# Performance work log

Hardware: AMD Instinct MI355X
Metric: run time of the kernel (lower is better)

## Reference

```python
import jax, jax.numpy as jnp
import numpy as np

DIM = 256
HEADS = 8
WH, WW = 7, 7
N = WH * WW
B_ = 2048


def _relative_position_index(wh, ww):
    coords = np.stack(np.meshgrid(np.arange(wh), np.arange(ww), indexing='ij'))  # (2,wh,ww)
    cf = coords.reshape(2, -1)  # (2, N)
    rel = cf[:, :, None] - cf[:, None, :]  # (2, N, N)
    rel = rel.transpose(1, 2, 0).astype(np.int32)
    rel[:, :, 0] += wh - 1
    rel[:, :, 1] += ww - 1
    rel[:, :, 0] *= 2 * ww - 1
    return rel.sum(-1)  # (N, N) int32


def setup_inputs() -> dict:
    key = jax.random.key(0)
    ks = jax.random.split(key, 7)
    return {
        'x1': jax.random.normal(ks[0], (B_, N, DIM), jnp.float32),
        'x2': jax.random.normal(ks[1], (B_, N, DIM), jnp.float32),
        'qkv_w': jax.random.normal(ks[2], (3 * DIM, DIM), jnp.float32) * 0.02,
        'qkv_b': jax.random.normal(ks[3], (3 * DIM,), jnp.float32) * 0.02,
        'proj_w': jax.random.normal(ks[4], (DIM, DIM), jnp.float32) * 0.02,
        'proj_b': jax.random.normal(ks[5], (DIM,), jnp.float32) * 0.02,
        'rpb_table': jax.random.normal(ks[6], ((2 * WH - 1) * (2 * WW - 1), HEADS), jnp.float32) * 0.02,
        'rel_index': jnp.asarray(_relative_position_index(WH, WW)),
    }


def reference(x1, x2, qkv_w, qkv_b, proj_w, proj_b, rpb_table, rel_index):
    B, n, C = x1.shape
    H = HEADS
    d = C // H
    scale = d ** (-0.5)

    def qkv(x):
        y = x @ qkv_w.T + qkv_b  # (B, N, 3C)
        y = y.reshape(B, n, 3, H, d).transpose(2, 0, 3, 1, 4)  # (3, B, H, N, d)
        return y[0], y[1], y[2]

    q1, _, _ = qkv(x1)
    _, k2, v2 = qkv(x2)

    attn = jnp.einsum('bhnd,bhmd->bhnm', q1 * scale, k2)  # (B, H, N, N)
    bias = rpb_table[rel_index]  # (N, N, H)
    attn = attn + bias.transpose(2, 0, 1)[None]  # broadcast over batch
    attn = jax.nn.softmax(attn, axis=-1)

    out = jnp.einsum('bhnm,bhmd->bhnd', attn, v2)  # (B, H, N, d)
    out = out.transpose(0, 2, 1, 3).reshape(B, n, C)
    return out @ proj_w.T + proj_b
```

## Files before the change

### kernel.cpp

```cpp
#include <hip/hip_runtime.h>
#include <hip/hip_bf16.h>

#define NTOK 49
#define NP 64
#define CDIM 256
#define NH 8
#define SCALE 0.17677669529663687f

#define SX_BYTES 32768
#define SV_BYTES 32768
#define SP_BYTES 16384

using f32x4  = __attribute__((ext_vector_type(4))) float;
using bf16x8 = __attribute__((ext_vector_type(8))) short;

__device__ __forceinline__ unsigned f2bf_u(float f) {
  union { float f; unsigned u; } c; c.f = f;
  return (c.u + 0x7fffu + ((c.u >> 16) & 1u)) >> 16;
}
__device__ __forceinline__ unsigned pk2(float a, float b) {
  return f2bf_u(a) | (f2bf_u(b) << 16);
}

__device__ __forceinline__ int sx_b(int row, int col) {
  return (row * 512 + col * 2) ^ ((row & 7) << 4);
}
__device__ __forceinline__ int sv_b(int feat, int tok) {
  return (feat * 128 + tok * 2) ^ ((feat & 7) << 4);
}
__device__ __forceinline__ int sp_b(int w, int row, int key) {
  return w * 2048 + ((row * 128 + key * 2) ^ ((row & 7) << 4));
}
__device__ __forceinline__ int so_b(int row, int col) {
  return (row * 512 + col * 4) ^ ((row & 7) << 4);
}

__global__ void prep_kernel(const float* __restrict__ qkv_w, const float* __restrict__ qkv_b,
                            const float* __restrict__ proj_w,
                            const float* __restrict__ rpb, const int* __restrict__ rel,
                            short* __restrict__ wqkv, short* __restrict__ wp,
                            float* __restrict__ bias_s, float* __restrict__ bias_att) {
  int i = blockIdx.x * 256 + threadIdx.x;
  if (i < 768 * 256) {
    int j = i >> 8;
    float v = qkv_w[i] * (j < 256 ? SCALE : 1.0f);
    wqkv[i] = (short)f2bf_u(v);
    return;
  }
  i -= 768 * 256;
  if (i < 256 * 256) { wp[i] = (short)f2bf_u(proj_w[i]); return; }
  i -= 256 * 256;
  if (i < 768) { bias_s[i] = qkv_b[i] * (i < 256 ? SCALE : 1.0f); return; }
  i -= 768;
  if (i < NH * NP * NP) {
    int h = i >> 12, rem = i & 4095, r = rem >> 6, c = rem & 63;
    float v;
    if (c >= NTOK)      v = -1e30f;
    else if (r >= NTOK) v = 0.0f;
    else                v = rpb[rel[r * NTOK + c] * NH + h];
    bias_att[i] = v;
  }
}

__device__ __forceinline__ void gemm32(const char* sxc, const short* __restrict__ wg,
                                       const float* __restrict__ bias,
                                       f32x4 acc[4][2], int w, int lr, int lg) {
  const short* wr0 = wg + (w * 32 + lr) * CDIM + lg * 8;
  const short* wr1 = wg + (w * 32 + 16 + lr) * CDIM + lg * 8;
  const float bv0 = bias[w * 32 + lr];
  const float bv1 = bias[w * 32 + 16 + lr];
  #pragma unroll
  for (int rt = 0; rt < 4; ++rt) {
    #pragma unroll
    for (int r = 0; r < 4; ++r) { acc[rt][0][r] = bv0; acc[rt][1][r] = bv1; }
  }
  #pragma unroll
  for (int k = 0; k < 8; ++k) {
    const bf16x8 b0 = *(const bf16x8*)(wr0 + k * 32);
    const bf16x8 b1 = *(const bf16x8*)(wr1 + k * 32);
    #pragma unroll
    for (int rt = 0; rt < 4; ++rt) {
      const bf16x8 af = *(const bf16x8*)(sxc + sx_b(rt * 16 + lr, k * 32 + lg * 8));
      acc[rt][0] = __builtin_amdgcn_mfma_f32_16x16x32_bf16(af, b0, acc[rt][0], 0, 0, 0);
      acc[rt][1] = __builtin_amdgcn_mfma_f32_16x16x32_bf16(af, b1, acc[rt][1], 0, 0, 0);
    }
  }
}

template <int NT>
__device__ __forceinline__ void stage_x(char* sxc, const float* __restrict__ xg, int tid) {
  #pragma unroll
  for (int it = 0; it < 4096 / NT; ++it) {
    const int i = tid + it * NT;
    const int row = i >> 6, c4 = i & 63;
    uint2 pkv = make_uint2(0u, 0u);
    if (row < NTOK) {
      const float4 v = *(const float4*)(xg + row * CDIM + c4 * 4);
      pkv.x = pk2(v.x, v.y); pkv.y = pk2(v.z, v.w);
    }
    *(uint2*)(sxc + sx_b(row, c4 * 4)) = pkv;
  }
}

#define IMG_STRIDE 98304

__global__ __launch_bounds__(512) __attribute__((amdgpu_waves_per_eu(4, 4)))
void qkv_kernel(const float* __restrict__ x1, const float* __restrict__ x2,
                const short* __restrict__ wqkv, const float* __restrict__ bias_s,
                char* __restrict__ img) {
  extern __shared__ char ldsc[];
  char* sxc = ldsc;
  char* stc = ldsc + 32768;

  const int tid = threadIdx.x;
  const int w = tid >> 6, lane = tid & 63;
  const int lr = lane & 15, lg = lane >> 4;
  const int b = blockIdx.x;
  char* wsb = img + (size_t)b * IMG_STRIDE;

  f32x4 acc[4][2];

  stage_x<512>(sxc, x1 + (size_t)b * NTOK * CDIM, tid);
  __syncthreads();

  gemm32(sxc, wqkv, bias_s, acc, w, lr, lg);
  #pragma unroll
  for (int rt = 0; rt < 4; ++rt)
    #pragma unroll
    for (int ct = 0; ct < 2; ++ct)
      #pragma unroll
      for (int r = 0; r < 4; ++r)
        *(short*)(stc + sx_b(rt * 16 + lg * 4 + r, w * 32 + ct * 16 + lr)) =
            (short)f2bf_u(acc[rt][ct][r]);
  __syncthreads();

  #pragma unroll
  for (int it = 0; it < 4; ++it) {
    const int i = tid + it * 512;
    *(float4*)(wsb + i * 16) = *(const float4*)(stc + i * 16);
  }
  stage_x<512>(sxc, x2 + (size_t)b * NTOK * CDIM, tid);
  __syncthreads();

  gemm32(sxc, wqkv + 512 * CDIM, bias_s + 512, acc, w, lr, lg);
  #pragma unroll
  for (int rt = 0; rt < 4; ++rt)
    #pragma unroll
    for (int ct = 0; ct < 2; ++ct) {
      uint2 pkv = make_uint2(pk2(acc[rt][ct][0], acc[rt][ct][1]),
                             pk2(acc[rt][ct][2], acc[rt][ct][3]));
      *(uint2*)(stc + sv_b(w * 32 + ct * 16 + lr, rt * 16 + lg * 4)) = pkv;
    }
  __syncthreads();

  #pragma unroll
  for (int it = 0; it < 4; ++it) {
    const int i = tid + it * 512;
    *(float4*)(wsb + 65536 + i * 16) = *(const float4*)(stc + i * 16);
  }
  gemm32(sxc, wqkv + 256 * CDIM, bias_s + 256, acc, w, lr, lg);
  __syncthreads();

  #pragma unroll
  for (int rt = 0; rt < 4; ++rt)
    #pragma unroll
    for (int ct = 0; ct < 2; ++ct)
      #pragma unroll
      for (int r = 0; r < 4; ++r)
        *(short*)(stc + sx_b(rt * 16 + lg * 4 + r, w * 32 + ct * 16 + lr)) =
            (short)f2bf_u(acc[rt][ct][r]);
  __syncthreads();

  #pragma unroll
  for (int it = 0; it < 4; ++it) {
    const int i = tid + it * 512;
    *(float4*)(wsb + 32768 + i * 16) = *(const float4*)(stc + i * 16);
  }
}

__global__ __launch_bounds__(256) __attribute__((amdgpu_waves_per_eu(4, 4)))
void attnproj_kernel(const char* __restrict__ img, const short* __restrict__ wp,
                     const float* __restrict__ proj_b, const float* __restrict__ bias_att,
                     float* __restrict__ out) {
  extern __shared__ char ldsc[];
  char* soc = ldsc;
  char* spc = ldsc + 32768;

  const int tid = threadIdx.x;
  const int w = tid >> 6, lane = tid & 63;
  const int lr = lane & 15, lg = lane >> 4;
  const int b = blockIdx.x;
  const char* qimg = img + (size_t)b * IMG_STRIDE;
  const char* kimg = qimg + 32768;
  const char* vimg = qimg + 65536;

  #pragma unroll
  for (int hh = 0; hh < 2; ++hh) {
    const int h = w * 2 + hh;
    bf16x8 kb[4];
    #pragma unroll
    for (int ct = 0; ct < 4; ++ct)
      kb[ct] = *(const bf16x8*)(kimg + sx_b(ct * 16 + lr, h * 32 + lg * 8));
    bf16x8 vb[2][2];
    #pragma unroll
    for (int kk = 0; kk < 2; ++kk)
      #pragma unroll
      for (int jt = 0; jt < 2; ++jt)
        vb[kk][jt] = *(const bf16x8*)(vimg + sv_b(h * 32 + jt * 16 + lr, kk * 32 + lg * 8));
    const float* bh = bias_att + h * NP * NP;

    #pragma unroll
    for (int qt = 0; qt < 4; ++qt) {
      const bf16x8 qa = *(const bf16x8*)(qimg + sx_b(qt * 16 + lr, h * 32 + lg * 8));
      f32x4 s[4];
      #pragma unroll
      for (int ct = 0; ct < 4; ++ct) {
        f32x4 sb;
        #pragma unroll
        for (int r = 0; r < 4; ++r) sb[r] = bh[(qt * 16 + lg * 4 + r) * NP + ct * 16 + lr];
        s[ct] = __builtin_amdgcn_mfma_f32_16x16x32_bf16(qa, kb[ct], sb, 0, 0, 0);
      }
      float mx[4], si[4];
      #pragma unroll
      for (int r = 0; r < 4; ++r) {
        float m = fmaxf(fmaxf(s[0][r], s[1][r]), fmaxf(s[2][r], s[3][r]));
        m = fmaxf(m, __shfl_xor(m, 1, 64));
        m = fmaxf(m, __shfl_xor(m, 2, 64));
        m = fmaxf(m, __shfl_xor(m, 4, 64));
        m = fmaxf(m, __shfl_xor(m, 8, 64));
        mx[r] = m;
      }
      #pragma unroll
      for (int ct = 0; ct < 4; ++ct)
        #pragma unroll
        for (int r = 0; r < 4; ++r)
          s[ct][r] = __expf(s[ct][r] - mx[r]);
      #pragma unroll
      for (int r = 0; r < 4; ++r) {
        float t = s[0][r] + s[1][r] + s[2][r] + s[3][r];
        t += __shfl_xor(t, 1, 64);
        t += __shfl_xor(t, 2, 64);
        t += __shfl_xor(t, 4, 64);
        t += __shfl_xor(t, 8, 64);
        si[r] = __builtin_amdgcn_rcpf(t);
      }
      #pragma unroll
      for (int ct = 0; ct < 4; ++ct)
        #pragma unroll
        for (int r = 0; r < 4; ++r)
          *(short*)(spc + sp_b(w, lg * 4 + r, ct * 16 + lr)) =
              (short)f2bf_u(s[ct][r] * si[r]);
      f32x4 oq[2];
      #pragma unroll
      for (int jt = 0; jt < 2; ++jt) { oq[jt][0] = 0; oq[jt][1] = 0; oq[jt][2] = 0; oq[jt][3] = 0; }
      #pragma unroll
      for (int kk = 0; kk < 2; ++kk) {
        const bf16x8 pa = *(const bf16x8*)(spc + sp_b(w, lr, kk * 32 + lg * 8));
        #pragma unroll
        for (int jt = 0; jt < 2; ++jt)
          oq[jt] = __builtin_amdgcn_mfma_f32_16x16x32_bf16(pa, vb[kk][jt], oq[jt], 0, 0, 0);
      }
      #pragma unroll
      for (int jt = 0; jt < 2; ++jt)
        #pragma unroll
        for (int r = 0; r < 4; ++r)
          *(short*)(soc + sx_b(qt * 16 + lg * 4 + r, h * 32 + jt * 16 + lr)) =
              (short)f2bf_u(oq[jt][r]);
    }
  }
  __syncthreads();

  float* og = out + (size_t)b * NTOK * CDIM;
  #pragma unroll
  for (int p = 0; p < 2; ++p) {
    const int c0 = w * 64 + p * 32;
    const short* wr0 = wp + (c0 + lr) * CDIM + lg * 8;
    const short* wr1 = wp + (c0 + 16 + lr) * CDIM + lg * 8;
    const float bv0 = proj_b[c0 + lr];
    const float bv1 = proj_b[c0 + 16 + lr];
    f32x4 acc[4][2];
    #pragma unroll
    for (int rt = 0; rt < 4; ++rt)
      #pragma unroll
      for (int r = 0; r < 4; ++r) { acc[rt][0][r] = bv0; acc[rt][1][r] = bv1; }
    #pragma unroll
    for (int k = 0; k < 8; ++k) {
      const bf16x8 b0 = *(const bf16x8*)(wr0 + k * 32);
      const bf16x8 b1 = *(const bf16x8*)(wr1 + k * 32);
      #pragma unroll
      for (int rt = 0; rt < 4; ++rt) {
        const bf16x8 af = *(const bf16x8*)(soc + sx_b(rt * 16 + lr, k * 32 + lg * 8));
        acc[rt][0] = __builtin_amdgcn_mfma_f32_16x16x32_bf16(af, b0, acc[rt][0], 0, 0, 0);
        acc[rt][1] = __builtin_amdgcn_mfma_f32_16x16x32_bf16(af, b1, acc[rt][1], 0, 0, 0);
      }
    }
    #pragma unroll
    for (int rt = 0; rt < 4; ++rt)
      #pragma unroll
      for (int r = 0; r < 4; ++r) {
        const int row = rt * 16 + lg * 4 + r;
        if (row < NTOK) {
          #pragma unroll
          for (int ct = 0; ct < 2; ++ct)
            og[row * CDIM + c0 + ct * 16 + lr] = acc[rt][ct][r];
        }
      }
  }
}

__global__ __launch_bounds__(512) __attribute__((amdgpu_waves_per_eu(4, 4)))
void fused_attn(const float* __restrict__ x1, const float* __restrict__ x2,
                const short* __restrict__ wqkv, const float* __restrict__ bias_s,
                const short* __restrict__ wp, const float* __restrict__ proj_b,
                const float* __restrict__ bias_att, float* __restrict__ out) {
  extern __shared__ char ldsc[];
  char* sxc = ldsc;
  char* svc = ldsc + SX_BYTES;
  char* spc = ldsc + SX_BYTES + SV_BYTES;

  const int tid = threadIdx.x;
  const int w = tid >> 6, lane = tid & 63;
  const int lr = lane & 15, lg = lane >> 4;
  const int b = blockIdx.x;
  const int r0 = (w >> 1) * 16;
  const int hb = (w & 1) * 4;

  stage_x<512>(sxc, x1 + (size_t)b * NTOK * CDIM, tid);
  __syncthreads();

  f32x4 acc[4][2];
  gemm32(sxc, wqkv, bias_s, acc, w, lr, lg);
  __syncthreads();
  #pragma unroll
  for (int rt = 0; rt < 4; ++rt)
    #pragma unroll
    for (int ct = 0; ct < 2; ++ct)
      #pragma unroll
      for (int r = 0; r < 4; ++r)
        *(short*)(sxc + sx_b(rt * 16 + lg * 4 + r, w * 32 + ct * 16 + lr)) =
            (short)f2bf_u(acc[rt][ct][r]);
  __syncthreads();

  bf16x8 qa[4];
  #pragma unroll
  for (int hh = 0; hh < 4; ++hh)
    qa[hh] = *(const bf16x8*)(sxc + sx_b(r0 + lr, (hb + hh) * 32 + lg * 8));
  __syncthreads();

  stage_x<512>(sxc, x2 + (size_t)b * NTOK * CDIM, tid);
  __syncthreads();

  gemm32(sxc, wqkv + 512 * CDIM, bias_s + 512, acc, w, lr, lg);
  #pragma unroll
  for (int rt = 0; rt < 4; ++rt)
    #pragma unroll
    for (int ct = 0; ct < 2; ++ct) {
      uint2 pkv = make_uint2(pk2(acc[rt][ct][0], acc[rt][ct][1]),
                             pk2(acc[rt][ct][2], acc[rt][ct][3]));
      *(uint2*)(svc + sv_b(w * 32 + ct * 16 + lr, rt * 16 + lg * 4)) = pkv;
    }

  gemm32(sxc, wqkv + 256 * CDIM, bias_s + 256, acc, w, lr, lg);
  __syncthreads();
  #pragma unroll
  for (int rt = 0; rt < 4; ++rt)
    #pragma unroll
    for (int ct = 0; ct < 2; ++ct)
      #pragma unroll
      for (int r = 0; r < 4; ++r)
        *(short*)(sxc + sx_b(rt * 16 + lg * 4 + r, w * 32 + ct * 16 + lr)) =
            (short)f2bf_u(acc[rt][ct][r]);
  __syncthreads();

  f32x4 oacc[4][2];
  #pragma unroll
  for (int hh = 0; hh < 4; ++hh)
    #pragma unroll
    for (int jt = 0; jt < 2; ++jt) {
      oacc[hh][jt][0] = 0; oacc[hh][jt][1] = 0; oacc[hh][jt][2] = 0; oacc[hh][jt][3] = 0;
    }

  #pragma unroll
  for (int hh = 0; hh < 4; ++hh) {
    const int h = hb + hh;
    const float* bh = bias_att + h * NP * NP + r0 * NP;
    f32x4 s[4];
    #pragma unroll
    for (int ct = 0; ct < 4; ++ct) {
      f32x4 sb;
      #pragma unroll
      for (int r = 0; r < 4; ++r) sb[r] = bh[(lg * 4 + r) * NP + ct * 16 + lr];
      const bf16x8 kb = *(const bf16x8*)(sxc + sx_b(ct * 16 + lr, h * 32 + lg * 8));
      s[ct] = __builtin_amdgcn_mfma_f32_16x16x32_bf16(qa[hh], kb, sb, 0, 0, 0);
    }
    float mx[4], si[4];
    #pragma unroll
    for (int r = 0; r < 4; ++r) {
      float m = fmaxf(fmaxf(s[0][r], s[1][r]), fmaxf(s[2][r], s[3][r]));
      m = fmaxf(m, __shfl_xor(m, 1, 64));
      m = fmaxf(m, __shfl_xor(m, 2, 64));
      m = fmaxf(m, __shfl_xor(m, 4, 64));
      m = fmaxf(m, __shfl_xor(m, 8, 64));
      mx[r] = m;
    }
    #pragma unroll
    for (int ct = 0; ct < 4; ++ct)
      #pragma unroll
      for (int r = 0; r < 4; ++r)
        s[ct][r] = __expf(s[ct][r] - mx[r]);
    #pragma unroll
    for (int r = 0; r < 4; ++r) {
      float t = s[0][r] + s[1][r] + s[2][r] + s[3][r];
      t += __shfl_xor(t, 1, 64);
      t += __shfl_xor(t, 2, 64);
      t += __shfl_xor(t, 4, 64);
      t += __shfl_xor(t, 8, 64);
      si[r] = __builtin_amdgcn_rcpf(t);
    }
    #pragma unroll
    for (int ct = 0; ct < 4; ++ct)
      #pragma unroll
      for (int r = 0; r < 4; ++r)
        *(short*)(spc + sp_b(w, lg * 4 + r, ct * 16 + lr)) =
            (short)f2bf_u(s[ct][r] * si[r]);
    #pragma unroll
    for (int kk = 0; kk < 2; ++kk) {
      const bf16x8 pa = *(const bf16x8*)(spc + sp_b(w, lr, kk * 32 + lg * 8));
      #pragma unroll
      for (int jt = 0; jt < 2; ++jt) {
        const bf16x8 vb = *(const bf16x8*)(svc + sv_b(h * 32 + jt * 16 + lr, kk * 32 + lg * 8));
        oacc[hh][jt] = __builtin_amdgcn_mfma_f32_16x16x32_bf16(pa, vb, oacc[hh][jt], 0, 0, 0);
      }
    }
  }

  __syncthreads();
  #pragma unroll
  for (int hh = 0; hh < 4; ++hh)
    #pragma unroll
    for (int jt = 0; jt < 2; ++jt)
      #pragma unroll
      for (int r = 0; r < 4; ++r)
        *(short*)(sxc + sx_b(r0 + lg * 4 + r, (hb + hh) * 32 + jt * 16 + lr)) =
            (short)f2bf_u(oacc[hh][jt][r]);
  __syncthreads();

  gemm32(sxc, wp, proj_b, acc, w, lr, lg);

  float* og = out + (size_t)b * NTOK * CDIM;
  #pragma unroll
  for (int half = 0; half < 2; ++half) {
    if ((w >> 2) == half) {
      const int wc = (w & 3) * 32;
      #pragma unroll
      for (int rt = 0; rt < 4; ++rt)
        #pragma unroll
        for (int ct = 0; ct < 2; ++ct)
          #pragma unroll
          for (int r = 0; r < 4; ++r)
            *(float*)(svc + so_b(rt * 16 + lg * 4 + r, wc + ct * 16 + lr)) = acc[rt][ct][r];
    }
    __syncthreads();
    for (int i = tid; i < NTOK * 32; i += 512) {
      const int row = i >> 5, c4 = i & 31;
      const float4 v = *(const float4*)(svc + so_b(row, c4 * 4));
      *(float4*)(og + row * CDIM + half * 128 + c4 * 4) = v;
    }
    __syncthreads();
  }
}

extern "C" void kernel_launch(void* const* d_in, const int* in_sizes, int n_in,
                              void* d_out, int out_size, void* d_ws, size_t ws_size,
                              hipStream_t stream) {
  const float* x1     = (const float*)d_in[0];
  const float* x2     = (const float*)d_in[1];
  const float* qkv_w  = (const float*)d_in[2];
  const float* qkv_b  = (const float*)d_in[3];
  const float* proj_w = (const float*)d_in[4];
  const float* proj_b = (const float*)d_in[5];
  const float* rpb    = (const float*)d_in[6];
  const int*   rel    = (const int*)d_in[7];

  char* ws = (char*)d_ws;
  short* wqkv     = (short*)ws;
  short* wp       = (short*)(ws + 393216);
  float* bias_s   = (float*)(ws + 524288);
  float* bias_att = (float*)(ws + 527360);
  char*  img      = ws + 658432;

  const int prep_total = 768 * 256 + 256 * 256 + 768 + NH * NP * NP;
  prep_kernel<<<(prep_total + 255) / 256, 256, 0, stream>>>(
      qkv_w, qkv_b, proj_w, rpb, rel, wqkv, wp, bias_s, bias_att);

  const int Bn = in_sizes[0] / (NTOK * CDIM);
  const size_t need = 658432 + (size_t)Bn * IMG_STRIDE;

  if (ws_size >= need) {
    (void)hipFuncSetAttribute((const void*)qkv_kernel,
                              hipFuncAttributeMaxDynamicSharedMemorySize, 65536);
    (void)hipFuncSetAttribute((const void*)attnproj_kernel,
                              hipFuncAttributeMaxDynamicSharedMemorySize, 40960);
    qkv_kernel<<<Bn, 512, 65536, stream>>>(x1, x2, wqkv, bias_s, img);
    attnproj_kernel<<<Bn, 256, 40960, stream>>>(img, wp, proj_b, bias_att, (float*)d_out);
  } else {
    const size_t shmem = SX_BYTES + SV_BYTES + SP_BYTES;
    (void)hipFuncSetAttribute((const void*)fused_attn,
                              hipFuncAttributeMaxDynamicSharedMemorySize, (int)shmem);
    fused_attn<<<Bn, 512, shmem, stream>>>(x1, x2, wqkv, bias_s, wp, proj_b, bias_att,
                                           (float*)d_out);
  }
}
```

Measured before the change: 290.8 us.

## Write QKV directly to global unswizzled, shrink qkv block, transpose bias table

The QKV kernel drops its LDS staging buffer and writes bf16 results straight to the global image in a plain unswizzled layout. It now runs with 256 threads, each wave covering two column slices, and uses 32KB of static LDS so more blocks can fit per CU. The attention bias table is stored transposed so each lane fetches its four bias values with one float4 load instead of four scalar loads. The risk is that the direct global writes are scattered 2-byte stores, which may coalesce worse than the earlier staged float4 copies.

```diff
diff --git a/kernel.cpp b/kernel.cpp
--- a/kernel.cpp
+++ b/kernel.cpp
@@ -10,6 +10,8 @@
 #define SX_BYTES 32768
 #define SV_BYTES 32768
 #define SP_BYTES 16384
+
+#define IMG_STRIDE 98304
 
 using f32x4  = __attribute__((ext_vector_type(4))) float;
 using bf16x8 = __attribute__((ext_vector_type(8))) short;
@@ -53,7 +55,7 @@
   if (i < 768) { bias_s[i] = qkv_b[i] * (i < 256 ? SCALE : 1.0f); return; }
   i -= 768;
   if (i < NH * NP * NP) {
-    int h = i >> 12, rem = i & 4095, r = rem >> 6, c = rem & 63;
+    int h = i >> 12, rem = i & 4095, c = rem >> 6, r = rem & 63;
     float v;
     if (c >= NTOK)      v = -1e30f;
     else if (r >= NTOK) v = 0.0f;
@@ -62,13 +64,13 @@
   }
 }
 
-__device__ __forceinline__ void gemm32(const char* sxc, const short* __restrict__ wg,
-                                       const float* __restrict__ bias,
-                                       f32x4 acc[4][2], int w, int lr, int lg) {
-  const short* wr0 = wg + (w * 32 + lr) * CDIM + lg * 8;
-  const short* wr1 = wg + (w * 32 + 16 + lr) * CDIM + lg * 8;
-  const float bv0 = bias[w * 32 + lr];
-  const float bv1 = bias[w * 32 + 16 + lr];
+__device__ __forceinline__ void gemm32c(const char* sxc, const short* __restrict__ wg,
+                                        const float* __restrict__ bias,
+                                        f32x4 acc[4][2], int col0, int lr, int lg) {
+  const short* wr0 = wg + (col0 + lr) * CDIM + lg * 8;
+  const short* wr1 = wg + (col0 + 16 + lr) * CDIM + lg * 8;
+  const float bv0 = bias[col0 + lr];
+  const float bv1 = bias[col0 + 16 + lr];
   #pragma unroll
   for (int rt = 0; rt < 4; ++rt) {
     #pragma unroll
@@ -102,79 +104,61 @@
   }
 }
 
-#define IMG_STRIDE 98304
-
-__global__ __launch_bounds__(512) __attribute__((amdgpu_waves_per_eu(4, 4)))
+__global__ __launch_bounds__(256) __attribute__((amdgpu_waves_per_eu(4, 4)))
 void qkv_kernel(const float* __restrict__ x1, const float* __restrict__ x2,
                 const short* __restrict__ wqkv, const float* __restrict__ bias_s,
                 char* __restrict__ img) {
-  extern __shared__ char ldsc[];
-  char* sxc = ldsc;
-  char* stc = ldsc + 32768;
-
+  __shared__ char sxc[SX_BYTES];
   const int tid = threadIdx.x;
   const int w = tid >> 6, lane = tid & 63;
   const int lr = lane & 15, lg = lane >> 4;
   const int b = blockIdx.x;
   char* wsb = img + (size_t)b * IMG_STRIDE;
 
+  stage_x<256>(sxc, x1 + (size_t)b * NTOK * CDIM, tid);
+  __syncthreads();
+
   f32x4 acc[4][2];
 
-  stage_x<512>(sxc, x1 + (size_t)b * NTOK * CDIM, tid);
-  __syncthreads();
-
-  gemm32(sxc, wqkv, bias_s, acc, w, lr, lg);
-  #pragma unroll
-  for (int rt = 0; rt < 4; ++rt)
-    #pragma unroll
-    for (int ct = 0; ct < 2; ++ct)
-      #pragma unroll
-      for (int r = 0; r < 4; ++r)
-        *(short*)(stc + sx_b(rt * 16 + lg * 4 + r, w * 32 + ct * 16 + lr)) =
-            (short)f2bf_u(acc[rt][ct][r]);
-  __syncthreads();
-
-  #pragma unroll
-  for (int it = 0; it < 4; ++it) {
-    const int i = tid + it * 512;
-    *(float4*)(wsb + i * 16) = *(const float4*)(stc + i * 16);
-  }
-  stage_x<512>(sxc, x2 + (size_t)b * NTOK * CDIM, tid);
-  __syncthreads();
-
-  gemm32(sxc, wqkv + 512 * CDIM, bias_s + 512, acc, w, lr, lg);
-  #pragma unroll
-  for (int rt = 0; rt < 4; ++rt)
-    #pragma unroll
-    for (int ct = 0; ct < 2; ++ct) {
-      uint2 pkv = make_uint2(pk2(acc[rt][ct][0], acc[rt][ct][1]),
-                             pk2(acc[rt][ct][2], acc[rt][ct][3]));
-      *(uint2*)(stc + sv_b(w * 32 + ct * 16 + lr, rt * 16 + lg * 4)) = pkv;
-    }
-  __syncthreads();
-
-  #pragma unroll
-  for (int it = 0; it < 4; ++it) {
-    const int i = tid + it * 512;
-    *(float4*)(wsb + 65536 + i * 16) = *(const float4*)(stc + i * 16);
-  }
-  gemm32(sxc, wqkv + 256 * CDIM, bias_s + 256, acc, w, lr, lg);
-  __syncthreads();
-
-  #pragma unroll
-  for (int rt = 0; rt < 4; ++rt)
-    #pragma unroll
-    for (int ct = 0; ct < 2; ++ct)
-      #pragma unroll
-      for (int r = 0; r < 4; ++r)
-        *(short*)(stc + sx_b(rt * 16 + lg * 4 + r, w * 32 + ct * 16 + lr)) =
-            (short)f2bf_u(acc[rt][ct][r]);
-  __syncthreads();
-
-  #pragma unroll
-  for (int it = 0; it < 4; ++it) {
-    const int i = tid + it * 512;
-    *(float4*)(wsb + 32768 + i * 16) = *(const float4*)(stc + i * 16);
+  #pragma unroll
+  for (int p = 0; p < 2; ++p) {
+    const int col0 = (p * 4 + w) * 32;
+    gemm32c(sxc, wqkv, bias_s, acc, col0, lr, lg);
+    #pragma unroll
+    for (int rt = 0; rt < 4; ++rt)
+      #pragma unroll
+      for (int ct = 0; ct < 2; ++ct)
+        #pragma unroll
+        for (int r = 0; r < 4; ++r)
+          *(short*)(wsb + (rt * 16 + lg * 4 + r) * 512 + (col0 + ct * 16 + lr) * 2) =
+              (short)f2bf_u(acc[rt][ct][r]);
+  }
+  __syncthreads();
+
+  stage_x<256>(sxc, x2 + (size_t)b * NTOK * CDIM, tid);
+  __syncthreads();
+
+  #pragma unroll
+  for (int p = 0; p < 2; ++p) {
+    const int col0 = (p * 4 + w) * 32;
+    gemm32c(sxc, wqkv + 512 * CDIM, bias_s + 512, acc, col0, lr, lg);
+    #pragma unroll
+    for (int rt = 0; rt < 4; ++rt)
+      #pragma unroll
+      for (int ct = 0; ct < 2; ++ct) {
+        uint2 pkv = make_uint2(pk2(acc[rt][ct][0], acc[rt][ct][1]),
+                               pk2(acc[rt][ct][2], acc[rt][ct][3]));
+        *(uint2*)(wsb + 65536 + (col0 + ct * 16 + lr) * 128 + (rt * 16 + lg * 4) * 2) = pkv;
+      }
+    gemm32c(sxc, wqkv + 256 * CDIM, bias_s + 256, acc, col0, lr, lg);
+    #pragma unroll
+    for (int rt = 0; rt < 4; ++rt)
+      #pragma unroll
+      for (int ct = 0; ct < 2; ++ct)
+        #pragma unroll
+        for (int r = 0; r < 4; ++r)
+          *(short*)(wsb + 32768 + (rt * 16 + lg * 4 + r) * 512 + (col0 + ct * 16 + lr) * 2) =
+              (short)f2bf_u(acc[rt][ct][r]);
   }
 }
 
@@ -200,24 +184,23 @@
     bf16x8 kb[4];
     #pragma unroll
     for (int ct = 0; ct < 4; ++ct)
-      kb[ct] = *(const bf16x8*)(kimg + sx_b(ct * 16 + lr, h * 32 + lg * 8));
+      kb[ct] = *(const bf16x8*)(kimg + (ct * 16 + lr) * 512 + (h * 32 + lg * 8) * 2);
     bf16x8 vb[2][2];
     #pragma unroll
     for (int kk = 0; kk < 2; ++kk)
       #pragma unroll
       for (int jt = 0; jt < 2; ++jt)
-        vb[kk][jt] = *(const bf16x8*)(vimg + sv_b(h * 32 + jt * 16 + lr, kk * 32 + lg * 8));
-    const float* bh = bias_att + h * NP * NP;
+        vb[kk][jt] = *(const bf16x8*)(vimg + (h * 32 + jt * 16 + lr) * 128 + (kk * 32 + lg * 8) * 2);
+    const float* bht = bias_att + h * NP * NP;
 
     #pragma unroll
     for (int qt = 0; qt < 4; ++qt) {
-      const bf16x8 qa = *(const bf16x8*)(qimg + sx_b(qt * 16 + lr, h * 32 + lg * 8));
+      const bf16x8 qa = *(const bf16x8*)(qimg + (qt * 16 + lr) * 512 + (h * 32 + lg * 8) * 2);
       f32x4 s[4];
       #pragma unroll
       for (int ct = 0; ct < 4; ++ct) {
-        f32x4 sb;
-        #pragma unroll
-        for (int r = 0; r < 4; ++r) sb[r] = bh[(qt * 16 + lg * 4 + r) * NP + ct * 16 + lr];
+        const float4 sbv = *(const float4*)(bht + (ct * 16 + lr) * NP + qt * 16 + lg * 4);
+        f32x4 sb; sb[0] = sbv.x; sb[1] = sbv.y; sb[2] = sbv.z; sb[3] = sbv.w;
         s[ct] = __builtin_amdgcn_mfma_f32_16x16x32_bf16(qa, kb[ct], sb, 0, 0, 0);
       }
       float mx[4], si[4];
@@ -329,7 +312,7 @@
   __syncthreads();
 
   f32x4 acc[4][2];
-  gemm32(sxc, wqkv, bias_s, acc, w, lr, lg);
+  gemm32c(sxc, wqkv, bias_s, acc, w * 32, lr, lg);
   __syncthreads();
   #pragma unroll
   for (int rt = 0; rt < 4; ++rt)
@@ -350,7 +333,7 @@
   stage_x<512>(sxc, x2 + (size_t)b * NTOK * CDIM, tid);
   __syncthreads();
 
-  gemm32(sxc, wqkv + 512 * CDIM, bias_s + 512, acc, w, lr, lg);
+  gemm32c(sxc, wqkv + 512 * CDIM, bias_s + 512, acc, w * 32, lr, lg);
   #pragma unroll
   for (int rt = 0; rt < 4; ++rt)
     #pragma unroll
@@ -360,7 +343,7 @@
       *(uint2*)(svc + sv_b(w * 32 + ct * 16 + lr, rt * 16 + lg * 4)) = pkv;
     }
 
-  gemm32(sxc, wqkv + 256 * CDIM, bias_s + 256, acc, w, lr, lg);
+  gemm32c(sxc, wqkv + 256 * CDIM, bias_s + 256, acc, w * 32, lr, lg);
   __syncthreads();
   #pragma unroll
   for (int rt = 0; rt < 4; ++rt)
@@ -383,13 +366,12 @@
   #pragma unroll
   for (int hh = 0; hh < 4; ++hh) {
     const int h = hb + hh;
-    const float* bh = bias_att + h * NP * NP + r0 * NP;
+    const float* bht = bias_att + h * NP * NP;
     f32x4 s[4];
     #pragma unroll
     for (int ct = 0; ct < 4; ++ct) {
-      f32x4 sb;
-      #pragma unroll
-      for (int r = 0; r < 4; ++r) sb[r] = bh[(lg * 4 + r) * NP + ct * 16 + lr];
+      const float4 sbv = *(const float4*)(bht + (ct * 16 + lr) * NP + r0 + lg * 4);
+      f32x4 sb; sb[0] = sbv.x; sb[1] = sbv.y; sb[2] = sbv.z; sb[3] = sbv.w;
       const bf16x8 kb = *(const bf16x8*)(sxc + sx_b(ct * 16 + lr, h * 32 + lg * 8));
       s[ct] = __builtin_amdgcn_mfma_f32_16x16x32_bf16(qa[hh], kb, sb, 0, 0, 0);
     }
@@ -445,7 +427,7 @@
             (short)f2bf_u(oacc[hh][jt][r]);
   __syncthreads();
 
-  gemm32(sxc, wp, proj_b, acc, w, lr, lg);
+  gemm32c(sxc, wp, proj_b, acc, w * 32, lr, lg);
 
   float* og = out + (size_t)b * NTOK * CDIM;
   #pragma unroll
@@ -497,11 +479,9 @@
   const size_t need = 658432 + (size_t)Bn * IMG_STRIDE;
 
   if (ws_size >= need) {
-    (void)hipFuncSetAttribute((const void*)qkv_kernel,
-                              hipFuncAttributeMaxDynamicSharedMemorySize, 65536);
     (void)hipFuncSetAttribute((const void*)attnproj_kernel,
                               hipFuncAttributeMaxDynamicSharedMemorySize, 40960);
-    qkv_kernel<<<Bn, 512, 65536, stream>>>(x1, x2, wqkv, bias_s, img);
+    qkv_kernel<<<Bn, 256, 0, stream>>>(x1, x2, wqkv, bias_s, img);
     attnproj_kernel<<<Bn, 256, 40960, stream>>>(img, wp, proj_b, bias_att, (float*)d_out);
   } else {
     const size_t shmem = SX_BYTES + SV_BYTES + SP_BYTES;
```

After: 498.6 us. 71.5% more time.
